# Optimization experiments

Measured on AMD Instinct MI355X. Metric: run time of the kernel, lower is better.

Reference implementation:

```python
import jax, jax.numpy as jnp
import numpy as np

BLK = 128          # stk blocking
HID = 1024         # hidden_size
FFN = 4096         # ffn_hidden_size per expert
NE = 8             # moe_num_experts
TOK = 8192         # padded tokens (multiple of BLK)


def setup_inputs() -> dict:
    key = jax.random.key(0)
    k1, k2, k3 = jax.random.split(key, 3)
    x = jax.random.normal(k1, (TOK, HID), dtype=jnp.float32)
    w1 = jax.random.normal(k2, (NE * FFN, HID), dtype=jnp.float32) * 0.02
    n_row_blocks = TOK // BLK          # 64
    cols_per_expert = FFN // BLK       # 32
    # dMoE topology: each token row-block is assigned one expert; its nonzero
    # column blocks are all ffn blocks of that expert.
    expert_assign = jax.random.randint(k3, (n_row_blocks,), 0, NE)
    row_indices = jnp.repeat(jnp.arange(n_row_blocks), cols_per_expert)
    column_indices = (expert_assign[:, None] * cols_per_expert
                      + jnp.arange(cols_per_expert)[None, :]).reshape(-1)
    return {
        "x": x,
        "w1": w1,
        "row_indices": row_indices.astype(jnp.int32),     # [nnz]
        "column_indices": column_indices.astype(jnp.int32),  # [nnz]
        "block": BLK,
    }


def reference(x, w1, row_indices, column_indices, block):
    # sdd(x, w1.T, topo): out block k = x_block[row_indices[k]] @ w1_block[column_indices[k]].T
    hid = x.shape[1]
    xb = x.reshape(-1, block, hid)    # [n_row_blocks, blk, hid]
    wb = w1.reshape(-1, block, hid)   # [n_col_blocks, blk, hid]
    # [nnz, blk, blk] block-sparse data of the output matrix
    return jnp.einsum('kbh,kch->kbc', xb[row_indices], wb[column_indices])
```

## Files before the change

### kernel.cpp

```cpp
#include <hip/hip_runtime.h>
#include <hip/hip_bf16.h>
#include <stdint.h>

#define HID 1024
#define BLKDIM 128
#define BKT 32
#define NKT (HID / BKT)
#define NBUF 3

using short8 = __attribute__((ext_vector_type(8))) short;
using f32x4  = __attribute__((ext_vector_type(4))) float;
using f32x4v = __attribute__((ext_vector_type(4))) float;

__device__ __forceinline__ uint32_t bfround(float f) {
    uint32_t u = __builtin_bit_cast(uint32_t, f);
    return (u + 0x7FFFu + ((u >> 16) & 1u)) >> 16;
}

__device__ __forceinline__ void gld16(const ushort* g, const ushort* lds_base) {
    __builtin_amdgcn_global_load_lds(
        (const __attribute__((address_space(1))) void*)g,
        (__attribute__((address_space(3))) void*)lds_base, 16, 0, 0);
}

__global__ __launch_bounds__(256)
void cvt_bf16_kernel(const float* __restrict__ src, uint4* __restrict__ dst, int n8) {
    int i = blockIdx.x * blockDim.x + threadIdx.x;
    if (i >= n8) return;
    const f32x4v* s = reinterpret_cast<const f32x4v*>(src) + (size_t)i * 2;
    f32x4v v0 = __builtin_nontemporal_load(s);
    f32x4v v1 = __builtin_nontemporal_load(s + 1);
    uint4 w;
    w.x = bfround(v0.x) | (bfround(v0.y) << 16);
    w.y = bfround(v0.z) | (bfround(v0.w) << 16);
    w.z = bfround(v1.x) | (bfround(v1.y) << 16);
    w.w = bfround(v1.z) | (bfround(v1.w) << 16);
    dst[i] = w;
}

__global__ void build_sched_kernel(const int* __restrict__ cind, int* __restrict__ perm) {
    __shared__ int srb[64];
    __shared__ int goff[9];
    const int t = threadIdx.x;
    if (t == 0) {
        int er[64], cnt[8], off[8];
        for (int e = 0; e < 8; ++e) cnt[e] = 0;
        for (int r = 0; r < 64; ++r) { er[r] = (cind[r * 32] >> 5) & 7; cnt[er[r]]++; }
        goff[0] = 0;
        for (int e = 0; e < 8; ++e) { goff[e + 1] = goff[e] + cnt[e]; off[e] = goff[e]; }
        for (int r = 0; r < 64; ++r) srb[off[er[r]]++] = r;
    }
    __syncthreads();
    for (int g = t; g < 1024; g += blockDim.x) {
        int e = 0;
        while (g >= goff[e + 1] * 16) ++e;
        const int ne = goff[e + 1] - goff[e];
        const int local = g - goff[e] * 16;
        const int j = local / ne;
        const int idx = local - j * ne;
        perm[g] = srb[goff[e] + idx] * 16 + j;
    }
}

__global__ __launch_bounds__(512, 4)
void sdd_pipe2_kernel(const ushort* __restrict__ xb, const ushort* __restrict__ wb,
                      const int* __restrict__ rind, const int* __restrict__ cind,
                      const int* __restrict__ perm,
                      float* __restrict__ out) {
    __shared__ ushort lds[NBUF * BLKDIM * BKT + NBUF * 2 * BLKDIM * BKT];

    int g = blockIdx.x;
    const int nwg = gridDim.x;
    if ((nwg & 7) == 0) {
        const int cpx = nwg >> 3;
        g = (g & 7) * cpx + (g >> 3);
    }
    g = perm[g];
    const int k0 = g * 2;
    const int r  = rind[k0];

    const int t = threadIdx.x;
    const int w = t >> 6;
    const int l = t & 63;

    ushort* sAb = lds;
    ushort* sBb = lds + NBUF * BLKDIM * BKT;

    const int unx   = (l & 7) ^ ((l >> 3) & 7);
    const int rin16 = 2 * (l >> 3) + (unx >> 2);
    const int kofs  = (unx & 3) * 8;

    const ushort* agb = xb + (size_t)(r * BLKDIM + w * 16 + rin16) * HID + kofs;
    const int cblk = cind[k0 + (w >> 2)];
    const ushort* bgb = wb + (size_t)(cblk * BLKDIM + (w & 3) * 32 + rin16) * HID + kofs;

    const int wr   = (w >> 2) * 64;
    const int wcol = (w & 3) * 64;
    const int ps_l = (((l >> 4) + ((l & 1) << 2)) ^ ((l & 15) >> 1)) * 8;
    const int rhalf = (l & 15) >> 1;

    int aoff[4], boff[4];
#pragma unroll
    for (int m = 0; m < 4; ++m) aoff[m] = (wr / 2 + m * 8 + rhalf) * 64 + ps_l;
#pragma unroll
    for (int n = 0; n < 4; ++n) boff[n] = (wcol / 2 + n * 8 + rhalf) * 64 + ps_l;

    f32x4 acc[4][4];
#pragma unroll
    for (int m = 0; m < 4; ++m)
#pragma unroll
        for (int n = 0; n < 4; ++n)
            acc[m][n] = (f32x4){0.f, 0.f, 0.f, 0.f};

    auto stage = [&](int b, int kt) {
        gld16(agb + kt * BKT, &sAb[b * 4096 + w * 512]);
        gld16(bgb + kt * BKT,                      &sBb[b * 8192 + (2 * w) * 512]);
        gld16(bgb + (size_t)16 * HID + kt * BKT,   &sBb[b * 8192 + (2 * w + 1) * 512]);
    };

    stage(0, 0);
    stage(1, 1);
    asm volatile("s_waitcnt vmcnt(3)" ::: "memory");
    __builtin_amdgcn_s_barrier();
    __builtin_amdgcn_sched_barrier(0);

    for (int kt = 0; kt < NKT; ++kt) {
        const int cur = kt % 3;
        const int nxt = (kt + 2) % 3;
        const bool pre = (kt + 2) < NKT;
        const ushort* sa = &sAb[cur * 4096];
        const ushort* sb = &sBb[cur * 8192];

        short8 aF[4], bF[4];
#pragma unroll
        for (int m = 0; m < 4; ++m)
            aF[m] = *reinterpret_cast<const short8*>(&sa[aoff[m]]);
#pragma unroll
        for (int n = 0; n < 4; ++n)
            bF[n] = *reinterpret_cast<const short8*>(&sb[boff[n]]);
        if (pre) stage(nxt, kt + 2);
        __builtin_amdgcn_s_setprio(1);
#pragma unroll
        for (int m = 0; m < 4; ++m)
#pragma unroll
            for (int n = 0; n < 4; ++n)
                acc[m][n] = __builtin_amdgcn_mfma_f32_16x16x32_bf16(aF[m], bF[n], acc[m][n], 0, 0, 0);
        __builtin_amdgcn_s_setprio(0);

        if (pre) asm volatile("s_waitcnt vmcnt(3)" ::: "memory");
        else     asm volatile("s_waitcnt vmcnt(0)" ::: "memory");
        __builtin_amdgcn_s_barrier();
        __builtin_amdgcn_sched_barrier(0);
    }

    const int blk = (w & 3) >> 1;
    float* op = out + (size_t)(k0 + blk) * (BLKDIM * BLKDIM);
    const int colbase = (wcol & 64) ? 64 : 0;
    float* scr = reinterpret_cast<float*>(lds) + w * 1152;

#pragma unroll
    for (int m = 0; m < 4; ++m) {
#pragma unroll
        for (int n = 0; n < 4; ++n)
#pragma unroll
            for (int j = 0; j < 4; ++j)
                scr[((l >> 4) * 4 + j) * 72 + n * 16 + (l & 15)] = acc[m][n][j];
#pragma unroll
        for (int rg = 0; rg < 4; ++rg) {
            const int tr = rg * 4 + (l >> 4);
            f32x4 v = *reinterpret_cast<const f32x4*>(&scr[tr * 72 + (l & 15) * 4]);
            __builtin_nontemporal_store(v,
                reinterpret_cast<f32x4*>(&op[(size_t)(wr + m * 16 + tr) * BLKDIM
                                             + colbase + (l & 15) * 4]));
        }
    }
}

__device__ __forceinline__ void store16f(ushort* dst, float4 v0, float4 v1, float4 v2, float4 v3) {
    uint4 w0, w1;
    w0.x = bfround(v0.x) | (bfround(v0.y) << 16);
    w0.y = bfround(v0.z) | (bfround(v0.w) << 16);
    w0.z = bfround(v1.x) | (bfround(v1.y) << 16);
    w0.w = bfround(v1.z) | (bfround(v1.w) << 16);
    w1.x = bfround(v2.x) | (bfround(v2.y) << 16);
    w1.y = bfround(v2.z) | (bfround(v2.w) << 16);
    w1.z = bfround(v3.x) | (bfround(v3.y) << 16);
    w1.w = bfround(v3.z) | (bfround(v3.w) << 16);
    uint4* d = reinterpret_cast<uint4*>(dst);
    d[0] = w0; d[1] = w1;
}

__global__ __launch_bounds__(256, 2)
void sdd_bf16_kernel(const float* __restrict__ x, const float* __restrict__ w1,
                     const int* __restrict__ rind, const int* __restrict__ cind,
                     float* __restrict__ out) {
    __shared__ ushort sA[2][BLKDIM * 32];
    __shared__ ushort sB[2][BLKDIM * 32];
    const int k = blockIdx.x;
    const int t = threadIdx.x;
    const int r = rind[k];
    const int c = cind[k];
    const float* Abase = x  + (size_t)r * BLKDIM * HID;
    const float* Bbase = w1 + (size_t)c * BLKDIM * HID;
    const int srow = t >> 1, shalf = t & 1;
    const float* aptr = Abase + (size_t)srow * HID + shalf * 16;
    const float* bptr = Bbase + (size_t)srow * HID + shalf * 16;
    const int soff = srow * 32 + shalf * 16;
    const int wv = t >> 6, lane = t & 63;
    const int wr = (wv >> 1) * 64, wc = (wv & 1) * 64;
    const int lr = lane & 15, lk = (lane >> 4) * 8;
    f32x4 acc[4][4];
#pragma unroll
    for (int m = 0; m < 4; ++m)
#pragma unroll
        for (int n = 0; n < 4; ++n) acc[m][n] = (f32x4){0.f, 0.f, 0.f, 0.f};
    float4 ra[4], rb[4];
#pragma unroll
    for (int i = 0; i < 4; ++i) {
        ra[i] = *reinterpret_cast<const float4*>(aptr + i * 4);
        rb[i] = *reinterpret_cast<const float4*>(bptr + i * 4);
    }
    store16f(&sA[0][soff], ra[0], ra[1], ra[2], ra[3]);
    store16f(&sB[0][soff], rb[0], rb[1], rb[2], rb[3]);
    __syncthreads();
    for (int kt = 0; kt < 32; ++kt) {
        const int cur = kt & 1;
        if (kt + 1 < 32) {
            const float* ap = aptr + (kt + 1) * 32;
            const float* bp = bptr + (kt + 1) * 32;
#pragma unroll
            for (int i = 0; i < 4; ++i) {
                ra[i] = *reinterpret_cast<const float4*>(ap + i * 4);
                rb[i] = *reinterpret_cast<const float4*>(bp + i * 4);
            }
        }
        const ushort* sa = sA[cur];
        const ushort* sb = sB[cur];
        short8 aF[4], bF[4];
#pragma unroll
        for (int m = 0; m < 4; ++m) aF[m] = *reinterpret_cast<const short8*>(&sa[(wr + m * 16 + lr) * 32 + lk]);
#pragma unroll
        for (int n = 0; n < 4; ++n) bF[n] = *reinterpret_cast<const short8*>(&sb[(wc + n * 16 + lr) * 32 + lk]);
#pragma unroll
        for (int m = 0; m < 4; ++m)
#pragma unroll
            for (int n = 0; n < 4; ++n)
                acc[m][n] = __builtin_amdgcn_mfma_f32_16x16x32_bf16(aF[m], bF[n], acc[m][n], 0, 0, 0);
        if (kt + 1 < 32) {
            store16f(&sA[cur ^ 1][soff], ra[0], ra[1], ra[2], ra[3]);
            store16f(&sB[cur ^ 1][soff], rb[0], rb[1], rb[2], rb[3]);
        }
        __syncthreads();
    }
    float* op = out + (size_t)k * (BLKDIM * BLKDIM);
    const int rbase = wr + (lane >> 4) * 4;
#pragma unroll
    for (int m = 0; m < 4; ++m)
#pragma unroll
        for (int n = 0; n < 4; ++n) {
            const int col = wc + n * 16 + lr;
#pragma unroll
            for (int j = 0; j < 4; ++j)
                op[(size_t)(rbase + m * 16 + j) * BLKDIM + col] = acc[m][n][j];
        }
}

extern "C" void kernel_launch(void* const* d_in, const int* in_sizes, int n_in,
                              void* d_out, int out_size, void* d_ws, size_t ws_size,
                              hipStream_t stream) {
    const float* x  = (const float*)d_in[0];
    const float* w1 = (const float*)d_in[1];
    const int* ri   = (const int*)d_in[2];
    const int* ci   = (const int*)d_in[3];
    float* out      = (float*)d_out;
    const int nnz   = in_sizes[2];
    const int nx    = in_sizes[0];
    const int nw    = in_sizes[1];

    const size_t need = ((size_t)nx + (size_t)nw) * sizeof(ushort) + 4096 * sizeof(int);
    if (ws_size >= need && nnz == 2048 && nx == 8388608) {
        ushort* xb = (ushort*)d_ws;
        ushort* wb = xb + nx;
        int* perm  = (int*)(wb + nw);
        const int nx8 = nx / 8, nw8 = nw / 8;
        hipLaunchKernelGGL(cvt_bf16_kernel, dim3((nx8 + 255) / 256), dim3(256), 0, stream,
                           x, (uint4*)xb, nx8);
        hipLaunchKernelGGL(cvt_bf16_kernel, dim3((nw8 + 255) / 256), dim3(256), 0, stream,
                           w1, (uint4*)wb, nw8);
        hipLaunchKernelGGL(build_sched_kernel, dim3(1), dim3(256), 0, stream, ci, perm);
        hipLaunchKernelGGL(sdd_pipe2_kernel, dim3(nnz / 2), dim3(512), 0, stream,
                           xb, wb, ri, ci, perm, out);
    } else {
        hipLaunchKernelGGL(sdd_bf16_kernel, dim3(nnz), dim3(256), 0, stream,
                           x, w1, ri, ci, out);
    }
}
```

Baseline: 135.9 us.

## Switch GEMM to 32x32x16 MFMA and fuse conversion with schedule build

The main kernel now uses 32x32x16 bf16 MFMA tiles (2x2 per wave) instead of 16x16x32 (4x4 per wave). This changes the LDS fragment addressing and the epilogue scratch layout. The bigger instruction is meant to cut MFMA issue count and LDS fragment reads per useful FLOP. The two bf16 conversion kernels and the schedule-build kernel are merged into one launch, which removes launch gaps. A risk is that block 0 both builds the permutation and converts data, and the schedule step has a serial section.

```diff
diff --git a/kernel.cpp b/kernel.cpp
--- a/kernel.cpp
+++ b/kernel.cpp
@@ -10,6 +10,7 @@
 
 using short8 = __attribute__((ext_vector_type(8))) short;
 using f32x4  = __attribute__((ext_vector_type(4))) float;
+using f32x16 = __attribute__((ext_vector_type(16))) float;
 using f32x4v = __attribute__((ext_vector_type(4))) float;
 
 __device__ __forceinline__ uint32_t bfround(float f) {
@@ -24,46 +25,61 @@
 }
 
 __global__ __launch_bounds__(256)
-void cvt_bf16_kernel(const float* __restrict__ src, uint4* __restrict__ dst, int n8) {
-    int i = blockIdx.x * blockDim.x + threadIdx.x;
-    if (i >= n8) return;
-    const f32x4v* s = reinterpret_cast<const f32x4v*>(src) + (size_t)i * 2;
-    f32x4v v0 = __builtin_nontemporal_load(s);
-    f32x4v v1 = __builtin_nontemporal_load(s + 1);
-    uint4 w;
-    w.x = bfround(v0.x) | (bfround(v0.y) << 16);
-    w.y = bfround(v0.z) | (bfround(v0.w) << 16);
-    w.z = bfround(v1.x) | (bfround(v1.y) << 16);
-    w.w = bfround(v1.z) | (bfround(v1.w) << 16);
-    dst[i] = w;
-}
-
-__global__ void build_sched_kernel(const int* __restrict__ cind, int* __restrict__ perm) {
-    __shared__ int srb[64];
-    __shared__ int goff[9];
+void cvt_sched_kernel(const float* __restrict__ x, const float* __restrict__ w1,
+                      uint4* __restrict__ xb, uint4* __restrict__ wb,
+                      int nx8, int nw8,
+                      const int* __restrict__ cind, int* __restrict__ perm) {
     const int t = threadIdx.x;
-    if (t == 0) {
-        int er[64], cnt[8], off[8];
-        for (int e = 0; e < 8; ++e) cnt[e] = 0;
-        for (int r = 0; r < 64; ++r) { er[r] = (cind[r * 32] >> 5) & 7; cnt[er[r]]++; }
-        goff[0] = 0;
-        for (int e = 0; e < 8; ++e) { goff[e + 1] = goff[e] + cnt[e]; off[e] = goff[e]; }
-        for (int r = 0; r < 64; ++r) srb[off[er[r]]++] = r;
-    }
-    __syncthreads();
-    for (int g = t; g < 1024; g += blockDim.x) {
-        int e = 0;
-        while (g >= goff[e + 1] * 16) ++e;
-        const int ne = goff[e + 1] - goff[e];
-        const int local = g - goff[e] * 16;
-        const int j = local / ne;
-        const int idx = local - j * ne;
-        perm[g] = srb[goff[e] + idx] * 16 + j;
+    if (blockIdx.x == 0) {
+        __shared__ int er[64], srb[64], goff[9];
+        if (t < 64) er[t] = (cind[t * 32] >> 5) & 7;
+        __syncthreads();
+        if (t == 0) {
+            int cnt[8], off[8];
+            for (int e = 0; e < 8; ++e) cnt[e] = 0;
+            for (int r = 0; r < 64; ++r) cnt[er[r]]++;
+            goff[0] = 0;
+            for (int e = 0; e < 8; ++e) { goff[e + 1] = goff[e] + cnt[e]; off[e] = goff[e]; }
+            for (int r = 0; r < 64; ++r) srb[off[er[r]]++] = r;
+        }
+        __syncthreads();
+        for (int g = t; g < 1024; g += 256) {
+            int e = 0;
+            while (g >= goff[e + 1] * 16) ++e;
+            const int ne = goff[e + 1] - goff[e];
+            const int local = g - goff[e] * 16;
+            const int j = local / ne;
+            const int idx = local - j * ne;
+            perm[g] = srb[goff[e] + idx] * 16 + j;
+        }
+    }
+    const int i = blockIdx.x * 256 + t;
+    if (i < nx8) {
+        const f32x4v* s = reinterpret_cast<const f32x4v*>(x) + (size_t)i * 2;
+        f32x4v v0 = __builtin_nontemporal_load(s);
+        f32x4v v1 = __builtin_nontemporal_load(s + 1);
+        uint4 w;
+        w.x = bfround(v0.x) | (bfround(v0.y) << 16);
+        w.y = bfround(v0.z) | (bfround(v0.w) << 16);
+        w.z = bfround(v1.x) | (bfround(v1.y) << 16);
+        w.w = bfround(v1.z) | (bfround(v1.w) << 16);
+        xb[i] = w;
+    } else if (i < nx8 + nw8) {
+        const int j = i - nx8;
+        const f32x4v* s = reinterpret_cast<const f32x4v*>(w1) + (size_t)j * 2;
+        f32x4v v0 = __builtin_nontemporal_load(s);
+        f32x4v v1 = __builtin_nontemporal_load(s + 1);
+        uint4 w;
+        w.x = bfround(v0.x) | (bfround(v0.y) << 16);
+        w.y = bfround(v0.z) | (bfround(v0.w) << 16);
+        w.z = bfround(v1.x) | (bfround(v1.y) << 16);
+        w.w = bfround(v1.z) | (bfround(v1.w) << 16);
+        wb[j] = w;
     }
 }
 
 __global__ __launch_bounds__(512, 4)
-void sdd_pipe2_kernel(const ushort* __restrict__ xb, const ushort* __restrict__ wb,
+void sdd_pipe3_kernel(const ushort* __restrict__ xb, const ushort* __restrict__ wb,
                       const int* __restrict__ rind, const int* __restrict__ cind,
                       const int* __restrict__ perm,
                       float* __restrict__ out) {
@@ -96,21 +112,26 @@
 
     const int wr   = (w >> 2) * 64;
     const int wcol = (w & 3) * 64;
-    const int ps_l = (((l >> 4) + ((l & 1) << 2)) ^ ((l & 15) >> 1)) * 8;
-    const int rhalf = (l & 15) >> 1;
-
-    int aoff[4], boff[4];
-#pragma unroll
-    for (int m = 0; m < 4; ++m) aoff[m] = (wr / 2 + m * 8 + rhalf) * 64 + ps_l;
-#pragma unroll
-    for (int n = 0; n < 4; ++n) boff[n] = (wcol / 2 + n * 8 + rhalf) * 64 + ps_l;
-
-    f32x4 acc[4][4];
-#pragma unroll
-    for (int m = 0; m < 4; ++m)
-#pragma unroll
-        for (int n = 0; n < 4; ++n)
-            acc[m][n] = (f32x4){0.f, 0.f, 0.f, 0.f};
+    const int lrow = l & 31;
+    const int r2   = lrow >> 1;
+    const int sub  = r2 & 7;
+    int aoff[2][2], boff[2][2];
+#pragma unroll
+    for (int f = 0; f < 2; ++f)
+#pragma unroll
+        for (int kk = 0; kk < 2; ++kk) {
+            const int ps = ((kk * 2 + (l >> 5) + 4 * (l & 1)) ^ sub) * 8;
+            aoff[f][kk] = (wr / 2   + f * 16 + r2) * 64 + ps;
+            boff[f][kk] = (wcol / 2 + f * 16 + r2) * 64 + ps;
+        }
+
+    f32x16 acc[2][2];
+#pragma unroll
+    for (int m = 0; m < 2; ++m)
+#pragma unroll
+        for (int n = 0; n < 2; ++n)
+#pragma unroll
+            for (int q = 0; q < 16; ++q) acc[m][n][q] = 0.f;
 
     auto stage = [&](int b, int kt) {
         gld16(agb + kt * BKT, &sAb[b * 4096 + w * 512]);
@@ -131,20 +152,24 @@
         const ushort* sa = &sAb[cur * 4096];
         const ushort* sb = &sBb[cur * 8192];
 
-        short8 aF[4], bF[4];
-#pragma unroll
-        for (int m = 0; m < 4; ++m)
-            aF[m] = *reinterpret_cast<const short8*>(&sa[aoff[m]]);
-#pragma unroll
-        for (int n = 0; n < 4; ++n)
-            bF[n] = *reinterpret_cast<const short8*>(&sb[boff[n]]);
+        short8 aF[2][2], bF[2][2];
+#pragma unroll
+        for (int f = 0; f < 2; ++f)
+#pragma unroll
+            for (int kk = 0; kk < 2; ++kk) {
+                aF[f][kk] = *reinterpret_cast<const short8*>(&sa[aoff[f][kk]]);
+                bF[f][kk] = *reinterpret_cast<const short8*>(&sb[boff[f][kk]]);
+            }
         if (pre) stage(nxt, kt + 2);
         __builtin_amdgcn_s_setprio(1);
 #pragma unroll
-        for (int m = 0; m < 4; ++m)
-#pragma unroll
-            for (int n = 0; n < 4; ++n)
-                acc[m][n] = __builtin_amdgcn_mfma_f32_16x16x32_bf16(aF[m], bF[n], acc[m][n], 0, 0, 0);
+        for (int kk = 0; kk < 2; ++kk)
+#pragma unroll
+            for (int m = 0; m < 2; ++m)
+#pragma unroll
+                for (int n = 0; n < 2; ++n)
+                    acc[m][n] = __builtin_amdgcn_mfma_f32_32x32x16_bf16(
+                        aF[m][kk], bF[n][kk], acc[m][n], 0, 0, 0);
         __builtin_amdgcn_s_setprio(0);
 
         if (pre) asm volatile("s_waitcnt vmcnt(3)" ::: "memory");
@@ -156,21 +181,23 @@
     const int blk = (w & 3) >> 1;
     float* op = out + (size_t)(k0 + blk) * (BLKDIM * BLKDIM);
     const int colbase = (wcol & 64) ? 64 : 0;
-    float* scr = reinterpret_cast<float*>(lds) + w * 1152;
-
-#pragma unroll
-    for (int m = 0; m < 4; ++m) {
-#pragma unroll
-        for (int n = 0; n < 4; ++n)
-#pragma unroll
-            for (int j = 0; j < 4; ++j)
-                scr[((l >> 4) * 4 + j) * 72 + n * 16 + (l & 15)] = acc[m][n][j];
-#pragma unroll
-        for (int rg = 0; rg < 4; ++rg) {
+    float* scr = reinterpret_cast<float*>(lds) + w * 2176;
+
+#pragma unroll
+    for (int m = 0; m < 2; ++m) {
+#pragma unroll
+        for (int n = 0; n < 2; ++n)
+#pragma unroll
+            for (int q = 0; q < 16; ++q) {
+                const int row32 = (q & 3) + 8 * (q >> 2) + 4 * (l >> 5);
+                scr[row32 * 68 + n * 32 + (l & 31)] = acc[m][n][q];
+            }
+#pragma unroll
+        for (int rg = 0; rg < 8; ++rg) {
             const int tr = rg * 4 + (l >> 4);
-            f32x4 v = *reinterpret_cast<const f32x4*>(&scr[tr * 72 + (l & 15) * 4]);
+            f32x4 v = *reinterpret_cast<const f32x4*>(&scr[tr * 68 + (l & 15) * 4]);
             __builtin_nontemporal_store(v,
-                reinterpret_cast<f32x4*>(&op[(size_t)(wr + m * 16 + tr) * BLKDIM
+                reinterpret_cast<f32x4*>(&op[(size_t)(wr + m * 32 + tr) * BLKDIM
                                              + colbase + (l & 15) * 4]));
         }
     }
@@ -283,12 +310,10 @@
         ushort* wb = xb + nx;
         int* perm  = (int*)(wb + nw);
         const int nx8 = nx / 8, nw8 = nw / 8;
-        hipLaunchKernelGGL(cvt_bf16_kernel, dim3((nx8 + 255) / 256), dim3(256), 0, stream,
-                           x, (uint4*)xb, nx8);
-        hipLaunchKernelGGL(cvt_bf16_kernel, dim3((nw8 + 255) / 256), dim3(256), 0, stream,
-                           w1, (uint4*)wb, nw8);
-        hipLaunchKernelGGL(build_sched_kernel, dim3(1), dim3(256), 0, stream, ci, perm);
-        hipLaunchKernelGGL(sdd_pipe2_kernel, dim3(nnz / 2), dim3(512), 0, stream,
+        const int ncvt = (nx8 + nw8 + 255) / 256;
+        hipLaunchKernelGGL(cvt_sched_kernel, dim3(ncvt), dim3(256), 0, stream,
+                           x, w1, (uint4*)xb, (uint4*)wb, nx8, nw8, ci, perm);
+        hipLaunchKernelGGL(sdd_pipe3_kernel, dim3(nnz / 2), dim3(512), 0, stream,
                            xb, wb, ri, ci, perm, out);
     } else {
         hipLaunchKernelGGL(sdd_bf16_kernel, dim3(nnz), dim3(256), 0, stream,
```

Result: faster. 131.6 us (-3.2%).

## Fuse fp32-to-bf16 conversion into the GEMM load path, drop pre-conversion kernels

Applied to the files above, without the earlier changes.

Removes the two separate bf16 conversion kernels and instead has the block-sparse GEMM load fp32 tiles from x and w1 into registers, round them to bf16, and write them into a double-buffered LDS layout. The full round trip of writing and re-reading bf16 copies of both inputs goes away. In exchange, the async global-to-LDS triple-buffer pipeline is replaced by register staging with a full vmcnt(0) wait each step. Each tile reads twice as many bytes as before, and x blocks are reread from fp32 by many workgroups. The schedule kernel now loads expert ids in parallel, and the epilogue scratch stride changes to 76.

```diff
diff --git a/kernel.cpp b/kernel.cpp
--- a/kernel.cpp
+++ b/kernel.cpp
@@ -6,7 +6,6 @@
 #define BLKDIM 128
 #define BKT 32
 #define NKT (HID / BKT)
-#define NBUF 3
 
 using short8 = __attribute__((ext_vector_type(8))) short;
 using f32x4  = __attribute__((ext_vector_type(4))) float;
@@ -17,35 +16,15 @@
     return (u + 0x7FFFu + ((u >> 16) & 1u)) >> 16;
 }
 
-__device__ __forceinline__ void gld16(const ushort* g, const ushort* lds_base) {
-    __builtin_amdgcn_global_load_lds(
-        (const __attribute__((address_space(1))) void*)g,
-        (__attribute__((address_space(3))) void*)lds_base, 16, 0, 0);
-}
-
-__global__ __launch_bounds__(256)
-void cvt_bf16_kernel(const float* __restrict__ src, uint4* __restrict__ dst, int n8) {
-    int i = blockIdx.x * blockDim.x + threadIdx.x;
-    if (i >= n8) return;
-    const f32x4v* s = reinterpret_cast<const f32x4v*>(src) + (size_t)i * 2;
-    f32x4v v0 = __builtin_nontemporal_load(s);
-    f32x4v v1 = __builtin_nontemporal_load(s + 1);
-    uint4 w;
-    w.x = bfround(v0.x) | (bfround(v0.y) << 16);
-    w.y = bfround(v0.z) | (bfround(v0.w) << 16);
-    w.z = bfround(v1.x) | (bfround(v1.y) << 16);
-    w.w = bfround(v1.z) | (bfround(v1.w) << 16);
-    dst[i] = w;
-}
-
 __global__ void build_sched_kernel(const int* __restrict__ cind, int* __restrict__ perm) {
-    __shared__ int srb[64];
-    __shared__ int goff[9];
+    __shared__ int er[64], srb[64], goff[9];
     const int t = threadIdx.x;
+    if (t < 64) er[t] = (cind[t * 32] >> 5) & 7;
+    __syncthreads();
     if (t == 0) {
-        int er[64], cnt[8], off[8];
+        int cnt[8], off[8];
         for (int e = 0; e < 8; ++e) cnt[e] = 0;
-        for (int r = 0; r < 64; ++r) { er[r] = (cind[r * 32] >> 5) & 7; cnt[er[r]]++; }
+        for (int r = 0; r < 64; ++r) cnt[er[r]]++;
         goff[0] = 0;
         for (int e = 0; e < 8; ++e) { goff[e + 1] = goff[e] + cnt[e]; off[e] = goff[e]; }
         for (int r = 0; r < 64; ++r) srb[off[er[r]]++] = r;
@@ -63,11 +42,11 @@
 }
 
 __global__ __launch_bounds__(512, 4)
-void sdd_pipe2_kernel(const ushort* __restrict__ xb, const ushort* __restrict__ wb,
+void sdd_fused_kernel(const float* __restrict__ x, const float* __restrict__ w1,
                       const int* __restrict__ rind, const int* __restrict__ cind,
                       const int* __restrict__ perm,
                       float* __restrict__ out) {
-    __shared__ ushort lds[NBUF * BLKDIM * BKT + NBUF * 2 * BLKDIM * BKT];
+    __shared__ ushort lds[2 * (BLKDIM * BKT + 2 * BLKDIM * BKT)];
 
     int g = blockIdx.x;
     const int nwg = gridDim.x;
@@ -83,16 +62,15 @@
     const int w = t >> 6;
     const int l = t & 63;
 
-    ushort* sAb = lds;
-    ushort* sBb = lds + NBUF * BLKDIM * BKT;
-
-    const int unx   = (l & 7) ^ ((l >> 3) & 7);
-    const int rin16 = 2 * (l >> 3) + (unx >> 2);
-    const int kofs  = (unx & 3) * 8;
-
-    const ushort* agb = xb + (size_t)(r * BLKDIM + w * 16 + rin16) * HID + kofs;
+    const int rin  = l >> 2;
+    const int q    = l & 3;
+    const int sub  = l >> 3;
+    const int wbase = sub * 64 + (((q + 4 * (rin & 1)) ^ sub) * 8);
+
+    const float* agx = x + (size_t)(r * BLKDIM + w * 16 + rin) * HID + q * 8;
     const int cblk = cind[k0 + (w >> 2)];
-    const ushort* bgb = wb + (size_t)(cblk * BLKDIM + (w & 3) * 32 + rin16) * HID + kofs;
+    const float* bgx0 = w1 + (size_t)(cblk * BLKDIM + (w & 3) * 32 + rin) * HID + q * 8;
+    const float* bgx1 = bgx0 + (size_t)16 * HID;
 
     const int wr   = (w >> 2) * 64;
     const int wcol = (w & 3) * 64;
@@ -112,25 +90,46 @@
         for (int n = 0; n < 4; ++n)
             acc[m][n] = (f32x4){0.f, 0.f, 0.f, 0.f};
 
-    auto stage = [&](int b, int kt) {
-        gld16(agb + kt * BKT, &sAb[b * 4096 + w * 512]);
-        gld16(bgb + kt * BKT,                      &sBb[b * 8192 + (2 * w) * 512]);
-        gld16(bgb + (size_t)16 * HID + kt * BKT,   &sBb[b * 8192 + (2 * w + 1) * 512]);
+    f32x4v ra0, ra1, rb0, rb1, rb2, rb3;
+
+    auto issue = [&](int kt) {
+        const float* pa  = agx  + kt * BKT;
+        const float* pb0 = bgx0 + kt * BKT;
+        const float* pb1 = bgx1 + kt * BKT;
+        ra0 = *reinterpret_cast<const f32x4v*>(pa);
+        ra1 = *reinterpret_cast<const f32x4v*>(pa + 4);
+        rb0 = *reinterpret_cast<const f32x4v*>(pb0);
+        rb1 = *reinterpret_cast<const f32x4v*>(pb0 + 4);
+        rb2 = *reinterpret_cast<const f32x4v*>(pb1);
+        rb3 = *reinterpret_cast<const f32x4v*>(pb1 + 4);
     };
-
-    stage(0, 0);
-    stage(1, 1);
-    asm volatile("s_waitcnt vmcnt(3)" ::: "memory");
-    __builtin_amdgcn_s_barrier();
-    __builtin_amdgcn_sched_barrier(0);
+    auto pack = [&](f32x4v v0, f32x4v v1) -> uint4 {
+        uint4 o;
+        o.x = bfround(v0.x) | (bfround(v0.y) << 16);
+        o.y = bfround(v0.z) | (bfround(v0.w) << 16);
+        o.z = bfround(v1.x) | (bfround(v1.y) << 16);
+        o.w = bfround(v1.z) | (bfround(v1.w) << 16);
+        return o;
+    };
+    auto write = [&](int b) {
+        ushort* base = lds + b * 12288;
+        *reinterpret_cast<uint4*>(&base[w * 512 + wbase])                  = pack(ra0, ra1);
+        *reinterpret_cast<uint4*>(&base[4096 + (2 * w) * 512 + wbase])     = pack(rb0, rb1);
+        *reinterpret_cast<uint4*>(&base[4096 + (2 * w + 1) * 512 + wbase]) = pack(rb2, rb3);
+    };
+
+    issue(0);
+    asm volatile("s_waitcnt vmcnt(0)" ::: "memory");
+    write(0);
+    __syncthreads();
 
     for (int kt = 0; kt < NKT; ++kt) {
-        const int cur = kt % 3;
-        const int nxt = (kt + 2) % 3;
-        const bool pre = (kt + 2) < NKT;
-        const ushort* sa = &sAb[cur * 4096];
-        const ushort* sb = &sBb[cur * 8192];
-
+        const int cur = kt & 1;
+        const bool pre = (kt + 1) < NKT;
+        if (pre) issue(kt + 1);
+
+        const ushort* sa = &lds[cur * 12288];
+        const ushort* sb = &lds[cur * 12288 + 4096];
         short8 aF[4], bF[4];
 #pragma unroll
         for (int m = 0; m < 4; ++m)
@@ -138,7 +137,6 @@
 #pragma unroll
         for (int n = 0; n < 4; ++n)
             bF[n] = *reinterpret_cast<const short8*>(&sb[boff[n]]);
-        if (pre) stage(nxt, kt + 2);
         __builtin_amdgcn_s_setprio(1);
 #pragma unroll
         for (int m = 0; m < 4; ++m)
@@ -147,16 +145,17 @@
                 acc[m][n] = __builtin_amdgcn_mfma_f32_16x16x32_bf16(aF[m], bF[n], acc[m][n], 0, 0, 0);
         __builtin_amdgcn_s_setprio(0);
 
-        if (pre) asm volatile("s_waitcnt vmcnt(3)" ::: "memory");
-        else     asm volatile("s_waitcnt vmcnt(0)" ::: "memory");
-        __builtin_amdgcn_s_barrier();
-        __builtin_amdgcn_sched_barrier(0);
+        if (pre) {
+            asm volatile("s_waitcnt vmcnt(0)" ::: "memory");
+            write(cur ^ 1);
+        }
+        __syncthreads();
     }
 
     const int blk = (w & 3) >> 1;
     float* op = out + (size_t)(k0 + blk) * (BLKDIM * BLKDIM);
     const int colbase = (wcol & 64) ? 64 : 0;
-    float* scr = reinterpret_cast<float*>(lds) + w * 1152;
+    float* scr = reinterpret_cast<float*>(lds) + w * 1216;
 
 #pragma unroll
     for (int m = 0; m < 4; ++m) {
@@ -164,11 +163,11 @@
         for (int n = 0; n < 4; ++n)
 #pragma unroll
             for (int j = 0; j < 4; ++j)
-                scr[((l >> 4) * 4 + j) * 72 + n * 16 + (l & 15)] = acc[m][n][j];
+                scr[((l >> 4) * 4 + j) * 76 + n * 16 + (l & 15)] = acc[m][n][j];
 #pragma unroll
         for (int rg = 0; rg < 4; ++rg) {
             const int tr = rg * 4 + (l >> 4);
-            f32x4 v = *reinterpret_cast<const f32x4*>(&scr[tr * 72 + (l & 15) * 4]);
+            f32x4 v = *reinterpret_cast<const f32x4*>(&scr[tr * 76 + (l & 15) * 4]);
             __builtin_nontemporal_store(v,
                 reinterpret_cast<f32x4*>(&op[(size_t)(wr + m * 16 + tr) * BLKDIM
                                              + colbase + (l & 15) * 4]));
@@ -277,19 +276,11 @@
     const int nx    = in_sizes[0];
     const int nw    = in_sizes[1];
 
-    const size_t need = ((size_t)nx + (size_t)nw) * sizeof(ushort) + 4096 * sizeof(int);
-    if (ws_size >= need && nnz == 2048 && nx == 8388608) {
-        ushort* xb = (ushort*)d_ws;
-        ushort* wb = xb + nx;
-        int* perm  = (int*)(wb + nw);
-        const int nx8 = nx / 8, nw8 = nw / 8;
-        hipLaunchKernelGGL(cvt_bf16_kernel, dim3((nx8 + 255) / 256), dim3(256), 0, stream,
-                           x, (uint4*)xb, nx8);
-        hipLaunchKernelGGL(cvt_bf16_kernel, dim3((nw8 + 255) / 256), dim3(256), 0, stream,
-                           w1, (uint4*)wb, nw8);
+    if (ws_size >= 1024 * sizeof(int) && nnz == 2048 && nx == 8388608 && nw == 33554432) {
+        int* perm = (int*)d_ws;
         hipLaunchKernelGGL(build_sched_kernel, dim3(1), dim3(256), 0, stream, ci, perm);
-        hipLaunchKernelGGL(sdd_pipe2_kernel, dim3(nnz / 2), dim3(512), 0, stream,
-                           xb, wb, ri, ci, perm, out);
+        hipLaunchKernelGGL(sdd_fused_kernel, dim3(nnz / 2), dim3(512), 0, stream,
+                           x, w1, ri, ci, perm, out);
     } else {
         hipLaunchKernelGGL(sdd_bf16_kernel, dim3(nnz), dim3(256), 0, stream,
                            x, w1, ri, ci, out);
```

After: 144.4 us. +6.2%, slower.
